# Kernel optimization log

Measured on AMD Instinct MI355X. Metric: run time of the kernel, lower is better.

The kernel has to match this reference:

```python
import jax, jax.numpy as jnp
import numpy as np

T, B, D, R = 1024, 32, 1024, 128

def _orth_cols(key, n, r):
    # mimic torch QR-based orthogonal init: Q[:, :r] of a random [n, r] matrix
    a = jax.random.normal(key, (n, r), dtype=jnp.float32)
    q, _ = jnp.linalg.qr(a)
    return q[:, :r]

def setup_inputs() -> dict:
    key = jax.random.key(0)
    ks = jax.random.split(key, 8)
    x = jax.random.normal(ks[0], (T, B, D), dtype=jnp.float32)
    z = jax.random.normal(ks[1], (T, B, D), dtype=jnp.float32)
    h0 = jnp.zeros((B, D), dtype=jnp.float32)
    U_h = _orth_cols(ks[2], D, R)
    V_h = _orth_cols(ks[3], D, R).T  # [R, D] with orthonormal rows
    U_x = _orth_cols(ks[4], D, R)
    V_x = _orth_cols(ks[5], D, R).T
    s_h = jnp.ones((R,), dtype=jnp.float32)
    s_x = jnp.ones((R,), dtype=jnp.float32)
    b = jnp.zeros((D,), dtype=jnp.float32)
    return {"x": x, "z": z, "h0": h0, "U_h": U_h, "V_h": V_h, "s_h": s_h,
            "U_x": U_x, "V_x": V_x, "s_x": s_x, "b": b}

def reference(x, z, h0, U_h, V_h, s_h, U_x, V_x, s_x, b):
    # Precompute V_x @ x_t for all timesteps: [T, B, R]
    Vx_all = jnp.einsum('tbd,rd->tbr', x, V_x)
    Ux_all = jnp.einsum('tbr,dr->tbd', s_x * Vx_all, U_x)  # input branch, no recurrence

    def step(h_prev, inp):
        Ux_t, z_t = inp
        Vh = h_prev @ V_h.T                 # [B, R]
        Uh = (s_h * Vh) @ U_h.T             # [B, D]
        h_new = jnp.tanh(Uh + Ux_t + b)
        out_t = h_new * jax.nn.silu(z_t)
        return h_new, (h_new, out_t)

    _, (hs, output) = jax.lax.scan(step, h0, (Ux_all, z))
    h = jnp.concatenate([h0[None], hs], axis=0)  # [T+1, B, D]
    return output, h
```

## Files before the change

### kernel.cpp

```cpp
#include <hip/hip_runtime.h>
#include <cstdint>

#define T_STEPS 1024
#define BATCH   32
#define DIM     1024
#define RANK    128
#define BD      (BATCH*DIM)
#define TBD     ((size_t)T_STEPS*BD)

typedef _Float16 half2v __attribute__((ext_vector_type(2)));

__device__ __forceinline__ float dot2f(uint32_t a, uint32_t b, float acc) {
#if __has_builtin(__builtin_amdgcn_fdot2)
  return __builtin_amdgcn_fdot2(__builtin_bit_cast(half2v, a),
                                __builtin_bit_cast(half2v, b), acc, false);
#else
  half2v xx = __builtin_bit_cast(half2v, a);
  half2v yy = __builtin_bit_cast(half2v, b);
  return acc + (float)xx[0]*(float)yy[0] + (float)xx[1]*(float)yy[1];
#endif
}

__device__ __forceinline__ float dot2x4(uint4 w, uint4 h, float acc) {
  acc = dot2f(w.x, h.x, acc); acc = dot2f(w.y, h.y, acc);
  acc = dot2f(w.z, h.z, acc); acc = dot2f(w.w, h.w, acc);
  return acc;
}

__device__ __forceinline__ uint16_t f16b(float x) {
  _Float16 h = (_Float16)x;
  return __builtin_bit_cast(unsigned short, h);
}
__device__ __forceinline__ uint32_t pack2(float a, float b) {
  return (uint32_t)f16b(a) | ((uint32_t)f16b(b) << 16);
}
__device__ __forceinline__ float fast_tanh(float x) {
  float e = __expf(2.0f*x);
  return 1.0f - 2.0f/(e + 1.0f);
}
__device__ __forceinline__ float fast_silu(float zz) {
  return zz / (1.0f + __expf(-zz));
}

__device__ __forceinline__ void pin4(uint4 &v) {
  asm volatile("" : "+v"(v.x), "+v"(v.y), "+v"(v.z), "+v"(v.w));
}

template<int CTRL>
__device__ __forceinline__ float dpp_xorf(float v) {
  int t = __builtin_amdgcn_mov_dpp(__builtin_bit_cast(int, v), CTRL, 0xf, 0xf, true);
  return __builtin_bit_cast(float, t);
}

__device__ __forceinline__ void lds_barrier() {
  asm volatile("s_waitcnt lgkmcnt(0)" ::: "memory");
  __builtin_amdgcn_s_barrier();
  __builtin_amdgcn_sched_barrier(0);
}

__global__ void prep_kernel(const float* __restrict__ Uh, const float* __restrict__ Vh,
                            const float* __restrict__ sh, const float* __restrict__ Ux,
                            const float* __restrict__ Vx, const float* __restrict__ sx,
                            const float* __restrict__ h0, uint32_t* __restrict__ ws32,
                            float* __restrict__ hout) {
  int i = blockIdx.x*blockDim.x + threadIdx.x;
  int n = gridDim.x*blockDim.x;
  for (int p = i; p < 65536; p += n) {
    int r = p >> 9, dp = p & 511;
    ws32[p] = pack2(Vh[r*1024 + 2*dp], Vh[r*1024 + 2*dp + 1]);
  }
  for (int p = i; p < 65536; p += n) {
    int d = p >> 6, k = p & 63;
    uint32_t w = pack2(Uh[d*128 + k]      * sh[k],
                       Uh[d*128 + 64 + k] * sh[64 + k]);
    if (k < 52) {
      int J = (k >> 2) + 13*(d & 1);
      ws32[65536 + J*2048 + (d >> 1)*4 + (k & 3)] = w;
    } else {
      ws32[118784 + d*12 + (k - 52)] = w;
    }
  }
  for (int p = i; p < 65536; p += n) {
    int r = p >> 9, dp = p & 511;
    ws32[131072 + p] = pack2(Vx[r*1024 + 2*dp], Vx[r*1024 + 2*dp + 1]);
  }
  for (int p = i; p < 65536; p += n) {
    int d = p >> 6, k = p & 63;
    uint32_t w = pack2(Ux[d*128 + 2*k]   * sx[2*k],
                       Ux[d*128 + 2*k+1] * sx[2*k+1]);
    ws32[196608 + (d >> 9)*32768 + (k >> 2)*2048 + (d & 511)*4 + (k & 3)] = w;
  }
  for (int p = i; p < BD; p += n) hout[p] = h0[p];
}

__global__ __attribute__((amdgpu_flat_work_group_size(512, 512),
                          amdgpu_waves_per_eu(2, 4)))
void inp_kernel(
    const float* __restrict__ x, const uint32_t* __restrict__ ws32,
    const float* __restrict__ bias, float* __restrict__ hout) {
  const int t = blockIdx.x;
  const int l = threadIdx.x;
  __shared__ __attribute__((aligned(16))) uint32_t xs[32*516];
  __shared__ __attribute__((aligned(16))) uint32_t svx[32*64];

  const float4* xg = (const float4*)(x + (size_t)t*BD);
  #pragma unroll
  for (int k = 0; k < 16; k++) {
    int i = l + 512*k;
    float4 v = xg[i];
    int bb = i >> 8;
    int d4 = i & 255;
    xs[bb*516 + d4*2]     = pack2(v.x, v.y);
    xs[bb*516 + d4*2 + 1] = pack2(v.z, v.w);
  }
  __syncthreads();

  const int rq = l >> 4;
  const int bq = l & 15;
  const uint4* xr0 = (const uint4*)(xs + bq*516);
  const uint4* xr1 = (const uint4*)(xs + (bq+16)*516);
  const uint4* wr0 = (const uint4*)(ws32 + 131072 + (4*rq    )*512);
  const uint4* wr1 = (const uint4*)(ws32 + 131072 + (4*rq + 1)*512);
  const uint4* wr2 = (const uint4*)(ws32 + 131072 + (4*rq + 2)*512);
  const uint4* wr3 = (const uint4*)(ws32 + 131072 + (4*rq + 3)*512);
  float a00=0.f,a01=0.f,a10=0.f,a11=0.f,a20=0.f,a21=0.f,a30=0.f,a31=0.f;
  #pragma unroll 2
  for (int J = 0; J < 128; J++) {
    uint4 x0 = xr0[J];
    uint4 x1 = xr1[J];
    uint4 w0 = wr0[J];
    uint4 w1 = wr1[J];
    uint4 w2 = wr2[J];
    uint4 w3 = wr3[J];
    a00 = dot2x4(w0, x0, a00); a01 = dot2x4(w0, x1, a01);
    a10 = dot2x4(w1, x0, a10); a11 = dot2x4(w1, x1, a11);
    a20 = dot2x4(w2, x0, a20); a21 = dot2x4(w2, x1, a21);
    a30 = dot2x4(w3, x0, a30); a31 = dot2x4(w3, x1, a31);
  }
  ((uint2*)(svx + bq*64))[rq]      = make_uint2(pack2(a00, a10), pack2(a20, a30));
  ((uint2*)(svx + (bq+16)*64))[rq] = make_uint2(pack2(a01, a11), pack2(a21, a31));
  __syncthreads();

  const uint4* svx4 = (const uint4*)svx;
  float accb[BATCH];
  #pragma unroll 1
  for (int dd = 0; dd < 2; dd++) {
    int d = l + dd*512;
    const uint4* uc = (const uint4*)(ws32 + 196608 + dd*32768);
    #pragma unroll
    for (int bi = 0; bi < BATCH; bi++) accb[bi] = 0.f;
    #pragma unroll
    for (int RP = 0; RP < 16; RP++) {
      uint4 w = uc[RP*512 + l];
      #pragma unroll
      for (int bi = 0; bi < BATCH; bi++) {
        uint4 sv = svx4[bi*16 + RP];
        accb[bi] = dot2f(w.x, sv.x, accb[bi]);
        accb[bi] = dot2f(w.y, sv.y, accb[bi]);
        accb[bi] = dot2f(w.z, sv.z, accb[bi]);
        accb[bi] = dot2f(w.w, sv.w, accb[bi]);
      }
    }
    float bv = bias[d];
    float* cslot = hout + (size_t)(t+1)*BD + d;
    #pragma unroll
    for (int bi = 0; bi < BATCH; bi++)
      cslot[(size_t)bi*DIM] = accb[bi] + bv;
  }
}

__global__ __attribute__((amdgpu_flat_work_group_size(512, 512),
                          amdgpu_waves_per_eu(2, 2)))
void rec_kernel(
    const uint32_t* __restrict__ ws32, const float* __restrict__ z,
    float* __restrict__ outb) {
  const int b  = blockIdx.x;
  const int l  = threadIdx.x;
  const int W  = l & 31;
  const int R8 = l >> 5;
  float* hout = outb + TBD;
  const uint4* vhw4  = (const uint4*)ws32;
  const uint4* uqs4  = (const uint4*)(ws32 + 65536);
  const uint4* ures4 = (const uint4*)(ws32 + 118784);

  __shared__ __attribute__((aligned(16))) uint4    vlds[6144];
  __shared__ __attribute__((aligned(16))) uint4    ulds[3072];
  __shared__ __attribute__((aligned(16))) uint4    hbuf[32*5];
  __shared__ __attribute__((aligned(16))) uint32_t svh32[64];

  uint4 vw[5][4];
  #pragma unroll
  for (int r = 0; r < 5; r++) {
    #pragma unroll
    for (int c = 0; c < 4; c++) vw[r][c] = vhw4[(8*R8 + r)*128 + W*4 + c];
  }
  #pragma unroll
  for (int r = 0; r < 5; r++) {
    #pragma unroll
    for (int c = 0; c < 4; c++) pin4(vw[r][c]);
  }
  #pragma unroll
  for (int rr = 0; rr < 3; rr++) {
    #pragma unroll
    for (int c = 0; c < 4; c++)
      vlds[R8*384 + rr*128 + c*32 + W] = vhw4[(8*R8 + 5 + rr)*128 + W*4 + c];
  }
  #pragma unroll
  for (int j = 0; j < 3; j++) {
    ulds[j*512 + l]     = ures4[(2*l)*3 + j];
    ulds[(3+j)*512 + l] = ures4[(2*l+1)*3 + j];
  }
  uint4 uq0[13], uq1[13];
  #pragma unroll
  for (int J = 0; J < 13; J++) {
    uq0[J] = uqs4[J*512 + l];
    uq1[J] = uqs4[(13+J)*512 + l];
  }
  {
    const float2 v = ((const float2*)(hout + (size_t)b*DIM))[l];
    ((uint32_t*)hbuf)[20*(l>>4) + (l&15)] = pack2(v.x, v.y);
  }
  __syncthreads();

  const float2* zp2 = (const float2*)(z + (size_t)b*DIM) + l;
  float2*       cp2 = (float2*)(hout + BD + (size_t)b*DIM) + l;
  float2*       op2 = (float2*)(outb + (size_t)b*DIM) + l;
  const uint4*  hb4  = hbuf + W*5;
  const uint4*  svh4 = (const uint4*)svh32;
  const int vbase = R8*384;

  #pragma unroll 1
  for (int t = 0; t < T_STEPS; t++) {
    float2 cc = *cp2;
    float2 zz = *zp2;

    float a[8] = {0.f,0.f,0.f,0.f,0.f,0.f,0.f,0.f};
    #pragma unroll
    for (int c = 0; c < 4; c++) {
      uint4 hvc = hb4[c];
      uint4 vA = vlds[vbase + c*32 + W];
      uint4 vB = vlds[vbase + 128 + c*32 + W];
      uint4 vC = vlds[vbase + 256 + c*32 + W];
      a[0] = dot2x4(vw[0][c], hvc, a[0]);
      a[1] = dot2x4(vw[1][c], hvc, a[1]);
      a[2] = dot2x4(vw[2][c], hvc, a[2]);
      a[3] = dot2x4(vw[3][c], hvc, a[3]);
      a[4] = dot2x4(vw[4][c], hvc, a[4]);
      a[5] = dot2x4(vA, hvc, a[5]);
      a[6] = dot2x4(vB, hvc, a[6]);
      a[7] = dot2x4(vC, hvc, a[7]);
    }
    float b4[4];
    {
      const bool s0 = (W & 1);
      #pragma unroll
      for (int i = 0; i < 4; i++) {
        float keep = s0 ? a[2*i+1] : a[2*i];
        float send = s0 ? a[2*i]   : a[2*i+1];
        b4[i] = keep + dpp_xorf<0xB1>(send);
      }
    }
    float c2[2];
    {
      const bool s1 = (W >> 1) & 1;
      #pragma unroll
      for (int i = 0; i < 2; i++) {
        float keep = s1 ? b4[2*i+1] : b4[2*i];
        float send = s1 ? b4[2*i]   : b4[2*i+1];
        c2[i] = keep + dpp_xorf<0x4E>(send);
      }
    }
    float s;
    {
      const bool s2 = (W >> 2) & 1;
      float keep = s2 ? c2[1] : c2[0];
      float send = s2 ? c2[0] : c2[1];
      s = keep + __shfl_xor(send, 4);
    }
    s += __shfl_xor(s, 8);
    s += __shfl_xor(s, 16);
    if (W < 8) {
      int row = 8*R8 + W;
      int idx = ((row & 63) << 1) | (row >> 6);
      ((uint16_t*)svh32)[idx] = f16b(s);
    }
    lds_barrier();

    float p0 = 0.f, p1 = 0.f;
    {
      uint4 sv0 = svh4[0], sv1 = svh4[1], sv2 = svh4[2], sv3 = svh4[3];
      p0 = dot2x4(uq0[0], sv0, p0); p1 = dot2x4(uq1[0], sv0, p1);
      p0 = dot2x4(uq0[1], sv1, p0); p1 = dot2x4(uq1[1], sv1, p1);
      p0 = dot2x4(uq0[2], sv2, p0); p1 = dot2x4(uq1[2], sv2, p1);
      p0 = dot2x4(uq0[3], sv3, p0); p1 = dot2x4(uq1[3], sv3, p1);
    }
    {
      uint4 sv0 = svh4[4], sv1 = svh4[5], sv2 = svh4[6], sv3 = svh4[7];
      p0 = dot2x4(uq0[4], sv0, p0); p1 = dot2x4(uq1[4], sv0, p1);
      p0 = dot2x4(uq0[5], sv1, p0); p1 = dot2x4(uq1[5], sv1, p1);
      p0 = dot2x4(uq0[6], sv2, p0); p1 = dot2x4(uq1[6], sv2, p1);
      p0 = dot2x4(uq0[7], sv3, p0); p1 = dot2x4(uq1[7], sv3, p1);
    }
    {
      uint4 sv0 = svh4[8], sv1 = svh4[9], sv2 = svh4[10], sv3 = svh4[11];
      p0 = dot2x4(uq0[8],  sv0, p0); p1 = dot2x4(uq1[8],  sv0, p1);
      p0 = dot2x4(uq0[9],  sv1, p0); p1 = dot2x4(uq1[9],  sv1, p1);
      p0 = dot2x4(uq0[10], sv2, p0); p1 = dot2x4(uq1[10], sv2, p1);
      p0 = dot2x4(uq0[11], sv3, p0); p1 = dot2x4(uq1[11], sv3, p1);
    }
    {
      uint4 sv0 = svh4[12], sv1 = svh4[13], sv2 = svh4[14], sv3 = svh4[15];
      uint4 u0b = ulds[0*512 + l], u0c = ulds[1*512 + l], u0d = ulds[2*512 + l];
      uint4 u1b = ulds[3*512 + l], u1c = ulds[4*512 + l], u1d = ulds[5*512 + l];
      p0 = dot2x4(uq0[12], sv0, p0); p1 = dot2x4(uq1[12], sv0, p1);
      p0 = dot2x4(u0b, sv1, p0); p1 = dot2x4(u1b, sv1, p1);
      p0 = dot2x4(u0c, sv2, p0); p1 = dot2x4(u1c, sv2, p1);
      p0 = dot2x4(u0d, sv3, p0); p1 = dot2x4(u1d, sv3, p1);
    }

    float hv0 = fast_tanh(p0 + cc.x);
    float hv1 = fast_tanh(p1 + cc.y);
    *cp2 = make_float2(hv0, hv1);
    ((uint32_t*)hbuf)[20*(l>>4) + (l&15)] = pack2(hv0, hv1);
    *op2 = make_float2(hv0 * fast_silu(zz.x), hv1 * fast_silu(zz.y));
    lds_barrier();

    cp2 += BD/2; zp2 += BD/2; op2 += BD/2;
  }
}

extern "C" void kernel_launch(void* const* d_in, const int* in_sizes, int n_in,
                              void* d_out, int out_size, void* d_ws, size_t ws_size,
                              hipStream_t stream) {
  const float* x  = (const float*)d_in[0];
  const float* z  = (const float*)d_in[1];
  const float* h0 = (const float*)d_in[2];
  const float* Uh = (const float*)d_in[3];
  const float* Vh = (const float*)d_in[4];
  const float* sh = (const float*)d_in[5];
  const float* Ux = (const float*)d_in[6];
  const float* Vx = (const float*)d_in[7];
  const float* sx = (const float*)d_in[8];
  const float* bb = (const float*)d_in[9];
  float* outb = (float*)d_out;
  uint32_t* ws32 = (uint32_t*)d_ws;

  prep_kernel<<<512, 256, 0, stream>>>(Uh, Vh, sh, Ux, Vx, sx, h0, ws32, outb + TBD);
  inp_kernel<<<T_STEPS, 512, 0, stream>>>(x, ws32, bb, outb + TBD);
  rec_kernel<<<BATCH, 512, 0, stream>>>(ws32, z, outb);
}
```

Baseline: 2.172 ms.

## Register-tile U_x projection in inp_kernel as 4 dims by 8 batches per thread

The second GEMM stage of the input kernel previously had each thread own one output dim across all 32 batches, reading every LDS vector once per batch. It now gives each thread 4 consecutive dims by 8 strided batches. Four weight vectors are loaded per rank chunk and each LDS read is reused across them. The U_x weight layout is reordered to match, and the svx LDS rows are padded from 64 to 68 words to avoid bank conflicts. In exchange, global stores are less coalesced, since each thread writes 4 adjacent floats per batch row and batches are spread across lanes.

```diff
diff --git a/kernel.cpp b/kernel.cpp
--- a/kernel.cpp
+++ b/kernel.cpp
@@ -85,10 +85,11 @@
     ws32[131072 + p] = pack2(Vx[r*1024 + 2*dp], Vx[r*1024 + 2*dp + 1]);
   }
   for (int p = i; p < 65536; p += n) {
-    int d = p >> 6, k = p & 63;
-    uint32_t w = pack2(Ux[d*128 + 2*k]   * sx[2*k],
-                       Ux[d*128 + 2*k+1] * sx[2*k+1]);
-    ws32[196608 + (d >> 9)*32768 + (k >> 2)*2048 + (d & 511)*4 + (k & 3)] = w;
+    int d = p >> 6, kw = p & 63;
+    uint32_t w = pack2(Ux[d*128 + 2*kw]   * sx[2*kw],
+                       Ux[d*128 + 2*kw+1] * sx[2*kw+1]);
+    int RP = kw >> 2, c = kw & 3;
+    ws32[196608 + (d >> 9)*32768 + RP*2048 + ((d >> 2) & 127)*16 + (d & 3)*4 + c] = w;
   }
   for (int p = i; p < BD; p += n) hout[p] = h0[p];
 }
@@ -101,7 +102,7 @@
   const int t = blockIdx.x;
   const int l = threadIdx.x;
   __shared__ __attribute__((aligned(16))) uint32_t xs[32*516];
-  __shared__ __attribute__((aligned(16))) uint32_t svx[32*64];
+  __shared__ __attribute__((aligned(16))) uint32_t svx[32*68];
 
   const float4* xg = (const float4*)(x + (size_t)t*BD);
   #pragma unroll
@@ -137,35 +138,47 @@
     a20 = dot2x4(w2, x0, a20); a21 = dot2x4(w2, x1, a21);
     a30 = dot2x4(w3, x0, a30); a31 = dot2x4(w3, x1, a31);
   }
-  ((uint2*)(svx + bq*64))[rq]      = make_uint2(pack2(a00, a10), pack2(a20, a30));
-  ((uint2*)(svx + (bq+16)*64))[rq] = make_uint2(pack2(a01, a11), pack2(a21, a31));
+  ((uint2*)svx)[bq*34 + rq]      = make_uint2(pack2(a00, a10), pack2(a20, a30));
+  ((uint2*)svx)[(bq+16)*34 + rq] = make_uint2(pack2(a01, a11), pack2(a21, a31));
   __syncthreads();
 
-  const uint4* svx4 = (const uint4*)svx;
-  float accb[BATCH];
+  const int bg = l & 3;
+  const int dg = l >> 2;
+  const uint4* sv4 = (const uint4*)svx;
+  float* cbase = hout + (size_t)(t+1)*BD;
   #pragma unroll 1
   for (int dd = 0; dd < 2; dd++) {
-    int d = l + dd*512;
-    const uint4* uc = (const uint4*)(ws32 + 196608 + dd*32768);
-    #pragma unroll
-    for (int bi = 0; bi < BATCH; bi++) accb[bi] = 0.f;
+    const uint4* uw = (const uint4*)(ws32 + 196608 + dd*32768);
+    float acc[4][8];
+    #pragma unroll
+    for (int k = 0; k < 4; k++)
+      #pragma unroll
+      for (int j = 0; j < 8; j++) acc[k][j] = 0.f;
     #pragma unroll
     for (int RP = 0; RP < 16; RP++) {
-      uint4 w = uc[RP*512 + l];
-      #pragma unroll
-      for (int bi = 0; bi < BATCH; bi++) {
-        uint4 sv = svx4[bi*16 + RP];
-        accb[bi] = dot2f(w.x, sv.x, accb[bi]);
-        accb[bi] = dot2f(w.y, sv.y, accb[bi]);
-        accb[bi] = dot2f(w.z, sv.z, accb[bi]);
-        accb[bi] = dot2f(w.w, sv.w, accb[bi]);
+      uint4 w0 = uw[RP*512 + dg*4 + 0];
+      uint4 w1 = uw[RP*512 + dg*4 + 1];
+      uint4 w2 = uw[RP*512 + dg*4 + 2];
+      uint4 w3 = uw[RP*512 + dg*4 + 3];
+      #pragma unroll
+      for (int j = 0; j < 8; j++) {
+        uint4 sv = sv4[(bg + 4*j)*17 + RP];
+        acc[0][j] = dot2x4(w0, sv, acc[0][j]);
+        acc[1][j] = dot2x4(w1, sv, acc[1][j]);
+        acc[2][j] = dot2x4(w2, sv, acc[2][j]);
+        acc[3][j] = dot2x4(w3, sv, acc[3][j]);
       }
     }
-    float bv = bias[d];
-    float* cslot = hout + (size_t)(t+1)*BD + d;
-    #pragma unroll
-    for (int bi = 0; bi < BATCH; bi++)
-      cslot[(size_t)bi*DIM] = accb[bi] + bv;
+    #pragma unroll
+    for (int k = 0; k < 4; k++) {
+      int d = dd*512 + 4*dg + k;
+      float bv = bias[d];
+      #pragma unroll
+      for (int j = 0; j < 8; j++) {
+        int b = bg + 4*j;
+        cbase[(size_t)b*DIM + d] = acc[k][j] + bv;
+      }
+    }
   }
 }
 
```

New measurement: 2.122 ms. 2.3% less time.
